# Performance work log

Hardware: AMD Instinct MI355X
Metric: run time of the kernel (lower is better)

The kernel has to match this reference:

```python
import jax, jax.numpy as jnp
import numpy as np

B, S, D, H = 4, 1024, 1024, 16
DH = D // H
K_SPARSE = 32
LAMBDA_MAX, ALPHA = 10.0, 5.0
SPARSE_THRESHOLD = 1.0


def setup_inputs() -> dict:
    key = jax.random.key(0)
    ks = jax.random.split(key, 12)
    x = jax.random.normal(ks[0], (B, S, D), dtype=jnp.float32)
    prior_mask = jax.random.bernoulli(ks[1], 0.1, (S, S))
    prior_indices = jax.random.randint(ks[2], (S, K_SPARSE), 0, S)
    prior_index_mask = jax.random.bernoulli(ks[3], 0.9, (S, K_SPARSE))
    prior_index_mask = prior_index_mask.at[:, 0].set(True)  # avoid all-masked rows
    u_prev = jax.random.normal(ks[4], (B, 1), dtype=jnp.float32)
    sc = 1.0 / np.sqrt(D)
    Wq = jax.random.normal(ks[5], (D, D), dtype=jnp.float32) * sc
    Wk = jax.random.normal(ks[6], (D, D), dtype=jnp.float32) * sc
    Wv = jax.random.normal(ks[7], (D, D), dtype=jnp.float32) * sc
    Wo = jax.random.normal(ks[8], (D, D), dtype=jnp.float32) * sc
    bq = jnp.zeros((D,), jnp.float32)
    bk = jnp.zeros((D,), jnp.float32)
    bv = jnp.zeros((D,), jnp.float32)
    bo = jnp.zeros((D,), jnp.float32)
    return {"x": x, "prior_mask": prior_mask, "prior_indices": prior_indices,
            "prior_index_mask": prior_index_mask, "u_prev": u_prev,
            "Wq": Wq, "bq": bq, "Wk": Wk, "bk": bk, "Wv": Wv, "bv": bv,
            "Wo": Wo, "bo": bo}


def reference(x, prior_mask, prior_indices, prior_index_mask, u_prev,
              Wq, bq, Wk, bk, Wv, bv, Wo, bo):
    Bb, Ss, Dd = x.shape
    scale = 1.0 / jnp.sqrt(jnp.asarray(DH, x.dtype))

    def proj(W, b):
        return (x @ W.T + b).reshape(Bb, Ss, H, DH).transpose(0, 2, 1, 3)  # [B,H,S,DH]

    Q, K, V = proj(Wq, bq), proj(Wk, bk), proj(Wv, bv)

    lam = LAMBDA_MAX * jnp.exp(-ALPHA * u_prev.reshape(Bb))  # [B]
    use_sparse = lam >= SPARSE_THRESHOLD                      # [B] bool

    # ---- dense branch: full SDPA with lambda-scaled prior bias ----
    scores = jnp.einsum('bhqd,bhkd->bhqk', Q, K) * scale      # [B,H,S,S]
    prior_bias = jnp.where(prior_mask[:Ss, :Ss], 0.0, -1.0).astype(x.dtype)
    bias = lam[:, None, None, None] * prior_bias[None, None]
    dense_out = jnp.einsum('bhqk,bhkd->bhqd',
                           jax.nn.softmax(scores + bias, axis=-1), V)

    # ---- sparse branch: gather-indexed SDPA over prior_indices ----
    idx = prior_indices[:Ss]                                   # [S,k]
    Kg = K[:, :, idx]                                          # [B,H,S,k,DH]
    Vg = V[:, :, idx]
    s_scores = jnp.einsum('bhsd,bhskd->bhsk', Q, Kg) * scale   # [B,H,S,k]
    s_scores = jnp.where(prior_index_mask[:Ss][None, None], s_scores,
                         jnp.asarray(-jnp.inf, x.dtype))
    sparse_out = jnp.einsum('bhsk,bhskd->bhsd',
                            jax.nn.softmax(s_scores, axis=-1), Vg)

    out = jnp.where(use_sparse[:, None, None, None], sparse_out, dense_out)
    out = out.transpose(0, 2, 1, 3).reshape(Bb, Ss, Dd)
    return out @ Wo.T + bo
```

## Files before the change

### kernel.cpp

```cpp
#include <hip/hip_runtime.h>
#include <hip/hip_bf16.h>
#include <cmath>

#define NB 4
#define NS 1024
#define ND 1024
#define NH 16
#define NDH 64
#define NKSP 32
#define SCALE 0.125f
#define LOG2E 1.44269504f
#define SCALE2 (SCALE * LOG2E)

typedef __attribute__((ext_vector_type(8))) short bf16x8;
typedef __attribute__((ext_vector_type(4))) float f32x4;
typedef unsigned long long u64;

#define AS1 __attribute__((address_space(1)))
#define AS3 __attribute__((address_space(3)))

__device__ __forceinline__ void gl_lds16(const void* g, void* l) {
    __builtin_amdgcn_global_load_lds((const AS1 void*)g, (AS3 void*)l, 16, 0, 0);
}

__device__ __forceinline__ ushort f2bf(float f) {
    union { __hip_bfloat16 h; ushort u; } cv;
    cv.h = __float2bfloat16(f);
    return cv.u;
}
__device__ __forceinline__ float bf2f(ushort u) {
    union { unsigned int i; float f; } cv;
    cv.i = ((unsigned int)u) << 16;
    return cv.f;
}
__device__ __forceinline__ float fexp2(float x) {
    return __builtin_amdgcn_exp2f(x);
}

__global__ __launch_bounds__(256)
void f2bf_multi(const float* __restrict__ x,
                const float* __restrict__ w0, const float* __restrict__ w1,
                const float* __restrict__ w2, const float* __restrict__ w3,
                const int* __restrict__ pm,
                ushort* __restrict__ xo,
                ushort* __restrict__ o0, ushort* __restrict__ o1,
                ushort* __restrict__ o2, ushort* __restrict__ o3,
                u64* __restrict__ bm)
{
    int y = blockIdx.y;
    if (y == 5) {
        int word = blockIdx.x * 4 + (threadIdx.x >> 6);
        int lane = threadIdx.x & 63;
        int row  = word >> 4, wcol = word & 15;
        int v = pm[(size_t)row * NS + wcol * 64 + lane];
        u64 b = __ballot(v != 0);
        if (lane == 0) bm[word] = b;
        return;
    }
    const float* src; ushort* dst; int nblk;
    if (y == 0)      { src = x;  dst = xo; nblk = 4096; }
    else if (y == 1) { src = w0; dst = o0; nblk = 1024; }
    else if (y == 2) { src = w1; dst = o1; nblk = 1024; }
    else if (y == 3) { src = w2; dst = o2; nblk = 1024; }
    else             { src = w3; dst = o3; nblk = 1024; }
    if (blockIdx.x >= (unsigned)nblk) return;
    int i = (blockIdx.x * 256 + threadIdx.x) * 4;
    float4 v = *(const float4*)&src[i];
    ushort4 o;
    o.x = f2bf(v.x); o.y = f2bf(v.y); o.z = f2bf(v.z); o.w = f2bf(v.w);
    *(ushort4*)&dst[i] = o;
}

__global__ __launch_bounds__(256)
void gemm_qkv(const ushort* __restrict__ xb,
              const ushort* __restrict__ Wqb, const ushort* __restrict__ Wkb,
              const ushort* __restrict__ Wvb,
              const float* __restrict__ bq, const float* __restrict__ bk,
              const float* __restrict__ bv,
              ushort* __restrict__ Qo, ushort* __restrict__ Ko,
              ushort* __restrict__ Vo, ushort* __restrict__ Vto)
{
    constexpr int K = ND;
    __shared__ __attribute__((aligned(16))) ushort As[128 * 32];
    __shared__ __attribute__((aligned(16))) ushort Bs[128 * 32];

    const int tid  = threadIdx.x;
    const int lane = tid & 63, w = tid >> 6;
    const int wm = w >> 1, wn = w & 1;
    const int which = blockIdx.x >> 3;
    const int n0 = (blockIdx.x & 7) * 128;
    const int m0 = blockIdx.y * 128;
    const int quad = lane >> 4, l16 = lane & 15;

    const ushort* W = (which == 0) ? Wqb : (which == 1) ? Wkb : Wvb;
    const float* bias = (which == 0) ? bq : (which == 1) ? bk : bv;
    ushort* Out = (which == 0) ? Qo : (which == 1) ? Ko : Vo;

    f32x4 acc[4][4] = {};

    for (int k0 = 0; k0 < K; k0 += 32) {
        __syncthreads();
#pragma unroll
        for (int u = 0; u < 2; ++u) {
            int t0 = u * 256 + w * 64;
            int t  = t0 + lane;
            int row = t >> 2, kc = (t & 3) * 8;
            gl_lds16(xb + (size_t)(m0 + row) * K + k0 + kc, &As[t0 * 8]);
            gl_lds16(W  + (size_t)(n0 + row) * K + k0 + kc, &Bs[t0 * 8]);
        }
        __syncthreads();

        bf16x8 af[4], bfr[4];
#pragma unroll
        for (int mt = 0; mt < 4; ++mt)
            af[mt] = *(const bf16x8*)&As[(wm*64 + mt*16 + l16) * 32 + quad*8];
#pragma unroll
        for (int nt = 0; nt < 4; ++nt)
            bfr[nt] = *(const bf16x8*)&Bs[(wn*64 + nt*16 + l16) * 32 + quad*8];
#pragma unroll
        for (int mt = 0; mt < 4; ++mt)
#pragma unroll
            for (int nt = 0; nt < 4; ++nt)
                acc[mt][nt] = __builtin_amdgcn_mfma_f32_16x16x32_bf16(
                    af[mt], bfr[nt], acc[mt][nt], 0, 0, 0);
    }

#pragma unroll
    for (int nt = 0; nt < 4; ++nt) {
        int n = n0 + wn*64 + nt*16 + l16;
        float bz = bias[n];
        int hh = n >> 6, dh = n & 63;
#pragma unroll
        for (int mt = 0; mt < 4; ++mt) {
#pragma unroll
            for (int rg = 0; rg < 4; ++rg) {
                int m = m0 + wm*64 + mt*16 + quad*4 + rg;
                int b = m >> 10, s = m & (NS - 1);
                ushort val = f2bf(acc[mt][nt][rg] + bz);
                Out[(((size_t)(b*NH + hh))*NS + s)*NDH + dh] = val;
                if (which == 2)
                    Vto[(((size_t)(b*NH + hh))*NDH + dh)*NS + s] = val;
            }
        }
    }
}

__global__ __launch_bounds__(256)
void gemm_out(const ushort* __restrict__ A, const ushort* __restrict__ W,
              const float* __restrict__ bias, float* __restrict__ Cout)
{
    constexpr int K = ND;
    __shared__ __attribute__((aligned(16))) ushort As[64 * 32];
    __shared__ __attribute__((aligned(16))) ushort Bs[128 * 32];

    const int tid  = threadIdx.x;
    const int lane = tid & 63, w = tid >> 6;
    const int wm = w & 1, wn = w >> 1;
    const int m0 = blockIdx.y * 64, n0 = blockIdx.x * 128;
    const int quad = lane >> 4, l16 = lane & 15;

    f32x4 acc[2][4] = {};

    for (int k0 = 0; k0 < K; k0 += 32) {
        __syncthreads();
        {
            int t0 = w * 64;
            int t  = t0 + lane;
            int row = t >> 2, kc = (t & 3) * 8;
            gl_lds16(A + (size_t)(m0 + row) * K + k0 + kc, &As[t0 * 8]);
        }
#pragma unroll
        for (int u = 0; u < 2; ++u) {
            int t0 = u * 256 + w * 64;
            int t  = t0 + lane;
            int row = t >> 2, kc = (t & 3) * 8;
            gl_lds16(W + (size_t)(n0 + row) * K + k0 + kc, &Bs[t0 * 8]);
        }
        __syncthreads();

        bf16x8 af[2], bfr[4];
#pragma unroll
        for (int mt = 0; mt < 2; ++mt)
            af[mt] = *(const bf16x8*)&As[(wm*32 + mt*16 + l16) * 32 + quad*8];
#pragma unroll
        for (int nt = 0; nt < 4; ++nt)
            bfr[nt] = *(const bf16x8*)&Bs[(wn*64 + nt*16 + l16) * 32 + quad*8];
#pragma unroll
        for (int mt = 0; mt < 2; ++mt)
#pragma unroll
            for (int nt = 0; nt < 4; ++nt)
                acc[mt][nt] = __builtin_amdgcn_mfma_f32_16x16x32_bf16(
                    af[mt], bfr[nt], acc[mt][nt], 0, 0, 0);
    }

#pragma unroll
    for (int nt = 0; nt < 4; ++nt) {
        int n = n0 + wn*64 + nt*16 + l16;
        float bz = bias[n];
#pragma unroll
        for (int mt = 0; mt < 2; ++mt) {
#pragma unroll
            for (int rg = 0; rg < 4; ++rg) {
                int m = m0 + wm*32 + mt*16 + quad*4 + rg;
                Cout[(size_t)m * ND + n] = acc[mt][nt][rg] + bz;
            }
        }
    }
}


#define STAGE(BUF, KT)                                                        \
    _Pragma("unroll")                                                         \
    for (int u = 0; u < 4; ++u) {                                             \
        int cb = w * 256 + u * 64;                                            \
        int c  = cb + lane;                                                   \
        const ushort* src;                                                    \
        if (w < 2) {                                                          \
            int row = c >> 3, sub = c & 7;                                    \
            src = Kh + (((size_t)((KT)*64 + row)) << 6)                       \
                     + ((sub ^ (row & 7)) << 3);                              \
        } else {                                                              \
            int c2 = c - 512;                                                 \
            int row = c2 >> 3, sub = c2 & 7;                                  \
            src = Vth + (size_t)row * NS + (KT)*64                            \
                      + ((sub ^ (row & 7)) << 3);                             \
        }                                                                     \
        gl_lds16(src, (ushort*)&KV[BUF][0][0] + (size_t)cb * 8);              \
    }

#define LOADKV(KF, VF, BUF)                                                   \
    _Pragma("unroll")                                                         \
    for (int nt = 0; nt < 4; ++nt)                                            \
        _Pragma("unroll")                                                     \
        for (int kk = 0; kk < 2; ++kk) {                                      \
            int rowk = nt*16 + l16;                                           \
            int ck = (kk*4 + quad) ^ (l16 & 7);                               \
            KF[nt][kk] = *(const bf16x8*)&KV[BUF][0][rowk*64 + ck*8];         \
            VF[nt][kk] = *(const bf16x8*)&KV[BUF][1][rowk*64 + ck*8];         \
        }

#define STEP(KT, KF, VF)                                                      \
    _Pragma("unroll")                                                         \
    for (int qh = 0; qh < 2; ++qh) {                                          \
        const int qrow = w*32 + qh*16 + l16;                                  \
        u64 wq = MW[(KT)*128 + qrow] >> (quad * 4);                           \
        f32x4 s_acc[4] = {};                                                  \
        __builtin_amdgcn_s_setprio(1);                                        \
        _Pragma("unroll")                                                     \
        for (int nt = 0; nt < 4; ++nt)                                        \
            _Pragma("unroll")                                                 \
            for (int kk = 0; kk < 2; ++kk)                                    \
                s_acc[nt] = __builtin_amdgcn_mfma_f32_16x16x32_bf16(          \
                    KF[nt][kk], qf[qh][kk], s_acc[nt], 0, 0, 0);              \
        __builtin_amdgcn_s_setprio(0);                                        \
        _Pragma("unroll")                                                     \
        for (int nt = 0; nt < 4; ++nt) {                                      \
            ushort4 pk;                                                       \
            float p0 = fexp2(fmaf(s_acc[nt][0], SCALE2,                       \
                 ((wq >> (nt*16 + 0)) & 1ULL) ? 0.f : nlam2));                \
            float p1 = fexp2(fmaf(s_acc[nt][1], SCALE2,                       \
                 ((wq >> (nt*16 + 1)) & 1ULL) ? 0.f : nlam2));                \
            float p2 = fexp2(fmaf(s_acc[nt][2], SCALE2,                       \
                 ((wq >> (nt*16 + 2)) & 1ULL) ? 0.f : nlam2));                \
            float p3 = fexp2(fmaf(s_acc[nt][3], SCALE2,                       \
                 ((wq >> (nt*16 + 3)) & 1ULL) ? 0.f : nlam2));                \
            pk.x = f2bf(p0); pk.y = f2bf(p1);                                 \
            pk.z = f2bf(p2); pk.w = f2bf(p3);                                 \
            *(ushort4*)&Ps[qrow*72 + nt*16 + quad*4] = pk;                    \
        }                                                                     \
        bf16x8 pf[2];                                                         \
        _Pragma("unroll")                                                     \
        for (int kk = 0; kk < 2; ++kk)                                        \
            pf[kk] = *(const bf16x8*)&Ps[qrow*72 + kk*32 + quad*8];           \
        __builtin_amdgcn_s_setprio(1);                                        \
        _Pragma("unroll")                                                     \
        for (int kk = 0; kk < 2; ++kk) {                                      \
            l_acc[qh] = __builtin_amdgcn_mfma_f32_16x16x32_bf16(              \
                pf[kk], ones.v, l_acc[qh], 0, 0, 0);                          \
            _Pragma("unroll")                                                 \
            for (int nt = 0; nt < 4; ++nt)                                    \
                o_acc[qh][nt] = __builtin_amdgcn_mfma_f32_16x16x32_bf16(      \
                    pf[kk], VF[nt][kk], o_acc[qh][nt], 0, 0, 0);              \
        }                                                                     \
        __builtin_amdgcn_s_setprio(0);                                        \
    }

__global__ __launch_bounds__(256, 2)
void attn_kernel(const ushort* __restrict__ Qb, const ushort* __restrict__ Kb,
                 const ushort* __restrict__ Vb, const ushort* __restrict__ Vt,
                 const u64* __restrict__ bm,
                 const int* __restrict__ pidx, const int* __restrict__ pimask,
                 const float* __restrict__ u_prev, ushort* __restrict__ OA)
{
    __shared__ __attribute__((aligned(16))) ushort Ps[128 * 72];
    __shared__ __attribute__((aligned(16))) u64    MW[16 * 128];
    __shared__ __attribute__((aligned(16))) ushort KV[2][2][64 * 64];

    const int tid  = threadIdx.x;
    const int lane = tid & 63, w = tid >> 6;
    const int quad = lane >> 4, l16 = lane & 15;

    const int id    = blockIdx.x;
    const int xcd   = id & 7;
    const int t5    = id >> 3;
    const int qtile = t5 & 7;
    const int head  = (t5 >> 3) * 8 + xcd;
    const int b = head >> 4, h = head & 15;
    const int s0 = qtile * 128;

    const float lam = 10.0f * __expf(-5.0f * u_prev[b]);
    const bool sparse = (lam >= 1.0f);

    const size_t bh = (size_t)b * NH + h;
    const ushort* Qh  = Qb + bh * NS * NDH;
    const ushort* Kh  = Kb + bh * NS * NDH;
    const ushort* Vh  = Vb + bh * NS * NDH;
    const ushort* Vth = Vt + bh * NDH * NS;

    if (!sparse) {
        const float nlam2 = -lam * LOG2E;

        STAGE(0, 0);
#pragma unroll
        for (int u = 0; u < 8; ++u) {
            int idx = u * 256 + tid;
            int row = idx >> 4, wd = idx & 15;
            MW[wd * 128 + row] = bm[(size_t)s0 * 16 + idx];
        }

        bf16x8 qf[2][2];
#pragma unroll
        for (int qh = 0; qh < 2; ++qh)
#pragma unroll
            for (int kk = 0; kk < 2; ++kk)
                qf[qh][kk] = *(const bf16x8*)
                    &Qh[(size_t)(s0 + w*32 + qh*16 + l16) * NDH + kk*32 + quad*8];

        union { bf16x8 v; ushort s[8]; } ones;
#pragma unroll
        for (int i = 0; i < 8; ++i) ones.s[i] = 0x3F80;

        f32x4 o_acc[2][4] = {};
        f32x4 l_acc[2] = {};

        __syncthreads();

        int cur = 0;
        for (int kt = 0; kt < 16; ++kt) {
            if (kt + 1 < 16) STAGE(cur ^ 1, kt + 1);
            bf16x8 kf[4][2], vf[4][2];
            LOADKV(kf, vf, cur);
            STEP(kt, kf, vf);
            __syncthreads();
            cur ^= 1;
        }

#pragma unroll
        for (int qh = 0; qh < 2; ++qh) {
            float inv[4];
#pragma unroll
            for (int rg = 0; rg < 4; ++rg) inv[rg] = 1.f / l_acc[qh][rg];
#pragma unroll
            for (int nt = 0; nt < 4; ++nt)
#pragma unroll
                for (int rg = 0; rg < 4; ++rg) {
                    int m = w*32 + qh*16 + quad*4 + rg;
                    OA[((size_t)b*NS + s0 + m)*ND + h*NDH + nt*16 + l16] =
                        f2bf(o_acc[qh][nt][rg] * inv[rg]);
                }
        }
    } else {
        const int r2  = lane & 15;
        const int cg  = lane >> 4;
#pragma unroll
        for (int qh = 0; qh < 2; ++qh) {
            const int row = w*32 + qh*16 + r2;

            float qreg[64];
            {
                const ushort* qp = Qh + (size_t)(s0 + row) * NDH;
#pragma unroll
                for (int c = 0; c < 8; ++c) {
                    union { bf16x8 v; ushort s[8]; } qv;
                    qv.v = *(const bf16x8*)(qp + c*8);
#pragma unroll
                    for (int j = 0; j < 8; ++j) qreg[c*8 + j] = bf2f(qv.s[j]);
                }
            }

            float sc[8];
#pragma unroll
            for (int jj = 0; jj < 8; ++jj) {
                int j  = cg*8 + jj;
                int mv = pimask[(size_t)(s0+row)*NKSP + j];
                if (mv) {
                    int kv = pidx[(size_t)(s0+row)*NKSP + j];
                    const ushort* krow = &Kh[(size_t)kv * NDH];
                    float acc = 0.f;
#pragma unroll
                    for (int c = 0; c < 8; ++c) {
                        union { bf16x8 v; ushort s[8]; } kk;
                        kk.v = *(const bf16x8*)(krow + c*8);
#pragma unroll
                        for (int jb = 0; jb < 8; ++jb)
                            acc = fmaf(qreg[c*8 + jb], bf2f(kk.s[jb]), acc);
                    }
                    sc[jj] = acc * SCALE;
                } else {
                    sc[jj] = -INFINITY;
                }
            }
            float mt = sc[0];
#pragma unroll
            for (int jj = 1; jj < 8; ++jj) mt = fmaxf(mt, sc[jj]);
            mt = fmaxf(mt, __shfl_xor(mt, 16));
            mt = fmaxf(mt, __shfl_xor(mt, 32));

            float psum = 0.f;
#pragma unroll
            for (int jj = 0; jj < 8; ++jj) {
                float p = __expf(sc[jj] - mt);
                psum += p;
                Ps[row * 72 + cg*8 + jj] = f2bf(p);
            }
            psum += __shfl_xor(psum, 16);
            psum += __shfl_xor(psum, 32);

            float o[16];
#pragma unroll
            for (int i = 0; i < 16; ++i) o[i] = 0.f;

            for (int j = 0; j < 32; ++j) {
                float p = bf2f(Ps[row * 72 + j]);
                if (p != 0.f) {
                    int kv = pidx[(size_t)(s0+row)*NKSP + j];
                    const ushort* vrow = &Vh[(size_t)kv * NDH + cg*16];
#pragma unroll
                    for (int c = 0; c < 2; ++c) {
                        union { bf16x8 v; ushort s[8]; } vv;
                        vv.v = *(const bf16x8*)(vrow + c*8);
#pragma unroll
                        for (int jb = 0; jb < 8; ++jb)
                            o[c*8 + jb] = fmaf(p, bf2f(vv.s[jb]), o[c*8 + jb]);
                    }
                }
            }

            float inv = 1.f / psum;
            ushort* op = OA + ((size_t)b*NS + s0 + row)*ND + h*NDH + cg*16;
#pragma unroll
            for (int i4 = 0; i4 < 4; ++i4) {
                ushort4 v;
                v.x = f2bf(o[i4*4+0]*inv); v.y = f2bf(o[i4*4+1]*inv);
                v.z = f2bf(o[i4*4+2]*inv); v.w = f2bf(o[i4*4+3]*inv);
                *(ushort4*)(op + i4*4) = v;
            }
        }
    }
}

extern "C" void kernel_launch(void* const* d_in, const int* in_sizes, int n_in,
                              void* d_out, int out_size, void* d_ws, size_t ws_size,
                              hipStream_t stream)
{
    const float* x      = (const float*)d_in[0];
    const int*   pmask  = (const int*)  d_in[1];
    const int*   pidx   = (const int*)  d_in[2];
    const int*   pimask = (const int*)  d_in[3];
    const float* u_prev = (const float*)d_in[4];
    const float* Wq     = (const float*)d_in[5];
    const float* bq     = (const float*)d_in[6];
    const float* Wk     = (const float*)d_in[7];
    const float* bk     = (const float*)d_in[8];
    const float* Wv     = (const float*)d_in[9];
    const float* bv     = (const float*)d_in[10];
    const float* Wo     = (const float*)d_in[11];
    const float* bo     = (const float*)d_in[12];
    float* out = (float*)d_out;

    const size_t QSZ = (size_t)NB * NH * NS * NDH;
    const size_t WSZ = (size_t)ND * ND;
    ushort* xb  = (ushort*)d_ws;
    ushort* Qw  = xb  + QSZ;
    ushort* Kw  = Qw  + QSZ;
    ushort* Vw  = Kw  + QSZ;
    ushort* Vtw = Vw  + QSZ;
    ushort* Awb = Vtw + QSZ;
    ushort* Wqb = Awb + QSZ;
    ushort* Wkb = Wqb + WSZ;
    ushort* Wvb = Wkb + WSZ;
    ushort* Wob = Wvb + WSZ;
    u64*    bmw = (u64*)(Wob + WSZ);

    f2bf_multi<<<dim3(4096, 6), 256, 0, stream>>>(
        x, Wq, Wk, Wv, Wo, pmask, xb, Wqb, Wkb, Wvb, Wob, bmw);

    gemm_qkv<<<dim3(24, 32), 256, 0, stream>>>(
        xb, Wqb, Wkb, Wvb, bq, bk, bv, Qw, Kw, Vw, Vtw);

    attn_kernel<<<512, 256, 0, stream>>>(
        Qw, Kw, Vw, Vtw, bmw, pidx, pimask, u_prev, Awb);

    gemm_out<<<dim3(ND/128, (NB*NS)/64), 256, 0, stream>>>(Awb, Wob, bo, out);
}
```

Before: 236.4 us.

## Split attention key range across wave pairs with smaller query tiles

The dense attention kernel now uses 64-row query tiles and 1024 blocks. Within each block the four waves are split into two query groups and two key halves: each key-half wave processes alternate key tiles and the partial O and row-sum accumulators are merged through shared memory at the end. V fragments are now read directly from global memory instead of being staged in LDS, and the sparse branch drops its data-dependent branches in favour of unconditional loads with masking. This raises parallelism and occupancy, at the cost of uncached global V reads, an extra reduction step, and a different block-to-head mapping.

New measurement: 226.0 us. 4.4% less time.

```diff
diff --git a/kernel.cpp b/kernel.cpp
--- a/kernel.cpp
+++ b/kernel.cpp
@@ -209,41 +209,36 @@
 }
 
 
-#define STAGE(BUF, KT)                                                        \
+#define STAGE(BUF, PT)                                                        \
     _Pragma("unroll")                                                         \
     for (int u = 0; u < 4; ++u) {                                             \
         int cb = w * 256 + u * 64;                                            \
         int c  = cb + lane;                                                   \
-        const ushort* src;                                                    \
-        if (w < 2) {                                                          \
-            int row = c >> 3, sub = c & 7;                                    \
-            src = Kh + (((size_t)((KT)*64 + row)) << 6)                       \
-                     + ((sub ^ (row & 7)) << 3);                              \
-        } else {                                                              \
-            int c2 = c - 512;                                                 \
-            int row = c2 >> 3, sub = c2 & 7;                                  \
-            src = Vth + (size_t)row * NS + (KT)*64                            \
-                      + ((sub ^ (row & 7)) << 3);                             \
-        }                                                                     \
-        gl_lds16(src, (ushort*)&KV[BUF][0][0] + (size_t)cb * 8);              \
-    }
-
-#define LOADKV(KF, VF, BUF)                                                   \
+        int wk2 = c >> 9, c2 = c & 511;                                       \
+        int row = c2 >> 3, sub = c2 & 7;                                      \
+        const ushort* src = Kh + (((size_t)(((PT) + wk2)*64 + row)) << 6)     \
+                               + ((sub ^ (row & 7)) << 3);                    \
+        gl_lds16(src, (ushort*)KK + (BUF)*8192 + (size_t)cb * 8);             \
+    }
+
+#define LOADKV(KF, VF, BUF, KT)                                               \
     _Pragma("unroll")                                                         \
     for (int nt = 0; nt < 4; ++nt)                                            \
         _Pragma("unroll")                                                     \
         for (int kk = 0; kk < 2; ++kk) {                                      \
             int rowk = nt*16 + l16;                                           \
             int ck = (kk*4 + quad) ^ (l16 & 7);                               \
-            KF[nt][kk] = *(const bf16x8*)&KV[BUF][0][rowk*64 + ck*8];         \
-            VF[nt][kk] = *(const bf16x8*)&KV[BUF][1][rowk*64 + ck*8];         \
+            KF[nt][kk] = *(const bf16x8*)                                     \
+                &((ushort*)KK)[(BUF)*8192 + wk*4096 + rowk*64 + ck*8];        \
+            VF[nt][kk] = *(const bf16x8*)                                     \
+                &Vth[(size_t)(nt*16 + l16) * NS + (KT)*64 + kk*32 + quad*8];  \
         }
 
 #define STEP(KT, KF, VF)                                                      \
     _Pragma("unroll")                                                         \
     for (int qh = 0; qh < 2; ++qh) {                                          \
-        const int qrow = w*32 + qh*16 + l16;                                  \
-        u64 wq = MW[(KT)*128 + qrow] >> (quad * 4);                           \
+        const int qrow = wq*32 + qh*16 + l16;                                 \
+        u64 wqm = MW[(KT)*64 + qrow] >> (quad * 4);                           \
         f32x4 s_acc[4] = {};                                                  \
         __builtin_amdgcn_s_setprio(1);                                        \
         _Pragma("unroll")                                                     \
@@ -257,21 +252,21 @@
         for (int nt = 0; nt < 4; ++nt) {                                      \
             ushort4 pk;                                                       \
             float p0 = fexp2(fmaf(s_acc[nt][0], SCALE2,                       \
-                 ((wq >> (nt*16 + 0)) & 1ULL) ? 0.f : nlam2));                \
+                 ((wqm >> (nt*16 + 0)) & 1ULL) ? 0.f : nlam2));               \
             float p1 = fexp2(fmaf(s_acc[nt][1], SCALE2,                       \
-                 ((wq >> (nt*16 + 1)) & 1ULL) ? 0.f : nlam2));                \
+                 ((wqm >> (nt*16 + 1)) & 1ULL) ? 0.f : nlam2));               \
             float p2 = fexp2(fmaf(s_acc[nt][2], SCALE2,                       \
-                 ((wq >> (nt*16 + 2)) & 1ULL) ? 0.f : nlam2));                \
+                 ((wqm >> (nt*16 + 2)) & 1ULL) ? 0.f : nlam2));               \
             float p3 = fexp2(fmaf(s_acc[nt][3], SCALE2,                       \
-                 ((wq >> (nt*16 + 3)) & 1ULL) ? 0.f : nlam2));                \
+                 ((wqm >> (nt*16 + 3)) & 1ULL) ? 0.f : nlam2));               \
             pk.x = f2bf(p0); pk.y = f2bf(p1);                                 \
             pk.z = f2bf(p2); pk.w = f2bf(p3);                                 \
-            *(ushort4*)&Ps[qrow*72 + nt*16 + quad*4] = pk;                    \
+            *(ushort4*)&Ps[wk][qrow*72 + nt*16 + quad*4] = pk;                \
         }                                                                     \
         bf16x8 pf[2];                                                         \
         _Pragma("unroll")                                                     \
         for (int kk = 0; kk < 2; ++kk)                                        \
-            pf[kk] = *(const bf16x8*)&Ps[qrow*72 + kk*32 + quad*8];           \
+            pf[kk] = *(const bf16x8*)&Ps[wk][qrow*72 + kk*32 + quad*8];       \
         __builtin_amdgcn_s_setprio(1);                                        \
         _Pragma("unroll")                                                     \
         for (int kk = 0; kk < 2; ++kk) {                                      \
@@ -292,21 +287,22 @@
                  const int* __restrict__ pidx, const int* __restrict__ pimask,
                  const float* __restrict__ u_prev, ushort* __restrict__ OA)
 {
-    __shared__ __attribute__((aligned(16))) ushort Ps[128 * 72];
-    __shared__ __attribute__((aligned(16))) u64    MW[16 * 128];
-    __shared__ __attribute__((aligned(16))) ushort KV[2][2][64 * 64];
+    __shared__ __attribute__((aligned(16))) ushort Ps[2][64 * 72];
+    __shared__ __attribute__((aligned(16))) u64    MW[16 * 64];
+    __shared__ __attribute__((aligned(16))) ushort KK[2][2][64 * 64];
 
     const int tid  = threadIdx.x;
     const int lane = tid & 63, w = tid >> 6;
     const int quad = lane >> 4, l16 = lane & 15;
+    const int wq = w & 1, wk = w >> 1;
 
     const int id    = blockIdx.x;
     const int xcd   = id & 7;
-    const int t5    = id >> 3;
-    const int qtile = t5 & 7;
-    const int head  = (t5 >> 3) * 8 + xcd;
-    const int b = head >> 4, h = head & 15;
-    const int s0 = qtile * 128;
+    const int b     = ((id >> 3) + (id >> 8)) & 3;
+    const int hb    = (id >> 5) & 1;
+    const int qtile = (id >> 6) & 15;
+    const int h     = hb * 8 + xcd;
+    const int s0    = qtile * 64;
 
     const float lam = 10.0f * __expf(-5.0f * u_prev[b]);
     const bool sparse = (lam >= 1.0f);
@@ -322,10 +318,10 @@
 
         STAGE(0, 0);
 #pragma unroll
-        for (int u = 0; u < 8; ++u) {
+        for (int u = 0; u < 4; ++u) {
             int idx = u * 256 + tid;
             int row = idx >> 4, wd = idx & 15;
-            MW[wd * 128 + row] = bm[(size_t)s0 * 16 + idx];
+            MW[wd * 64 + row] = bm[(size_t)s0 * 16 + idx];
         }
 
         bf16x8 qf[2][2];
@@ -334,7 +330,7 @@
 #pragma unroll
             for (int kk = 0; kk < 2; ++kk)
                 qf[qh][kk] = *(const bf16x8*)
-                    &Qh[(size_t)(s0 + w*32 + qh*16 + l16) * NDH + kk*32 + quad*8];
+                    &Qh[(size_t)(s0 + wq*32 + qh*16 + l16) * NDH + kk*32 + quad*8];
 
         union { bf16x8 v; ushort s[8]; } ones;
 #pragma unroll
@@ -346,35 +342,65 @@
         __syncthreads();
 
         int cur = 0;
-        for (int kt = 0; kt < 16; ++kt) {
-            if (kt + 1 < 16) STAGE(cur ^ 1, kt + 1);
+        for (int t = 0; t < 8; ++t) {
+            if (t + 1 < 8) STAGE(cur ^ 1, 2*(t + 1));
             bf16x8 kf[4][2], vf[4][2];
-            LOADKV(kf, vf, cur);
+            const int kt = 2*t + wk;
+            LOADKV(kf, vf, cur, kt);
             STEP(kt, kf, vf);
             __syncthreads();
             cur ^= 1;
         }
 
-#pragma unroll
-        for (int qh = 0; qh < 2; ++qh) {
-            float inv[4];
-#pragma unroll
-            for (int rg = 0; rg < 4; ++rg) inv[rg] = 1.f / l_acc[qh][rg];
-#pragma unroll
-            for (int nt = 0; nt < 4; ++nt)
-#pragma unroll
-                for (int rg = 0; rg < 4; ++rg) {
-                    int m = w*32 + qh*16 + quad*4 + rg;
-                    OA[((size_t)b*NS + s0 + m)*ND + h*NDH + nt*16 + l16] =
-                        f2bf(o_acc[qh][nt][rg] * inv[rg]);
-                }
+        float* POUT = (float*)KK;
+        if (wk == 1) {
+#pragma unroll
+            for (int qh = 0; qh < 2; ++qh) {
+#pragma unroll
+                for (int nt = 0; nt < 4; ++nt)
+#pragma unroll
+                    for (int rg = 0; rg < 4; ++rg)
+                        POUT[(wq*40 + qh*16 + nt*4 + rg)*64 + lane] =
+                            o_acc[qh][nt][rg];
+#pragma unroll
+                for (int rg = 0; rg < 4; ++rg)
+                    POUT[(wq*40 + 32 + qh*4 + rg)*64 + lane] = l_acc[qh][rg];
+            }
+        }
+        __syncthreads();
+        if (wk == 0) {
+#pragma unroll
+            for (int qh = 0; qh < 2; ++qh) {
+#pragma unroll
+                for (int nt = 0; nt < 4; ++nt)
+#pragma unroll
+                    for (int rg = 0; rg < 4; ++rg)
+                        o_acc[qh][nt][rg] +=
+                            POUT[(wq*40 + qh*16 + nt*4 + rg)*64 + lane];
+#pragma unroll
+                for (int rg = 0; rg < 4; ++rg)
+                    l_acc[qh][rg] += POUT[(wq*40 + 32 + qh*4 + rg)*64 + lane];
+            }
+#pragma unroll
+            for (int qh = 0; qh < 2; ++qh) {
+                float inv[4];
+#pragma unroll
+                for (int rg = 0; rg < 4; ++rg) inv[rg] = 1.f / l_acc[qh][rg];
+#pragma unroll
+                for (int nt = 0; nt < 4; ++nt)
+#pragma unroll
+                    for (int rg = 0; rg < 4; ++rg) {
+                        int m = wq*32 + qh*16 + quad*4 + rg;
+                        OA[((size_t)b*NS + s0 + m)*ND + h*NDH + nt*16 + l16] =
+                            f2bf(o_acc[qh][nt][rg] * inv[rg]);
+                    }
+            }
         }
     } else {
         const int r2  = lane & 15;
         const int cg  = lane >> 4;
-#pragma unroll
-        for (int qh = 0; qh < 2; ++qh) {
-            const int row = w*32 + qh*16 + r2;
+        {
+            const int row = w*16 + r2;
 
             float qreg[64];
             {
@@ -393,22 +419,18 @@
             for (int jj = 0; jj < 8; ++jj) {
                 int j  = cg*8 + jj;
                 int mv = pimask[(size_t)(s0+row)*NKSP + j];
-                if (mv) {
-                    int kv = pidx[(size_t)(s0+row)*NKSP + j];
-                    const ushort* krow = &Kh[(size_t)kv * NDH];
-                    float acc = 0.f;
-#pragma unroll
-                    for (int c = 0; c < 8; ++c) {
-                        union { bf16x8 v; ushort s[8]; } kk;
-                        kk.v = *(const bf16x8*)(krow + c*8);
-#pragma unroll
-                        for (int jb = 0; jb < 8; ++jb)
-                            acc = fmaf(qreg[c*8 + jb], bf2f(kk.s[jb]), acc);
-                    }
-                    sc[jj] = acc * SCALE;
-                } else {
-                    sc[jj] = -INFINITY;
+                int kv = pidx[(size_t)(s0+row)*NKSP + j];
+                const ushort* krow = &Kh[(size_t)kv * NDH];
+                float acc = 0.f;
+#pragma unroll
+                for (int c = 0; c < 8; ++c) {
+                    union { bf16x8 v; ushort s[8]; } kk;
+                    kk.v = *(const bf16x8*)(krow + c*8);
+#pragma unroll
+                    for (int jb = 0; jb < 8; ++jb)
+                        acc = fmaf(qreg[c*8 + jb], bf2f(kk.s[jb]), acc);
                 }
+                sc[jj] = mv ? acc * SCALE : -INFINITY;
             }
             float mt = sc[0];
 #pragma unroll
@@ -421,7 +443,7 @@
             for (int jj = 0; jj < 8; ++jj) {
                 float p = __expf(sc[jj] - mt);
                 psum += p;
-                Ps[row * 72 + cg*8 + jj] = f2bf(p);
+                Ps[0][row * 72 + cg*8 + jj] = f2bf(p);
             }
             psum += __shfl_xor(psum, 16);
             psum += __shfl_xor(psum, 32);
@@ -430,19 +452,18 @@
 #pragma unroll
             for (int i = 0; i < 16; ++i) o[i] = 0.f;
 
+#pragma unroll 4
             for (int j = 0; j < 32; ++j) {
-                float p = bf2f(Ps[row * 72 + j]);
-                if (p != 0.f) {
-                    int kv = pidx[(size_t)(s0+row)*NKSP + j];
-                    const ushort* vrow = &Vh[(size_t)kv * NDH + cg*16];
-#pragma unroll
-                    for (int c = 0; c < 2; ++c) {
-                        union { bf16x8 v; ushort s[8]; } vv;
-                        vv.v = *(const bf16x8*)(vrow + c*8);
-#pragma unroll
-                        for (int jb = 0; jb < 8; ++jb)
-                            o[c*8 + jb] = fmaf(p, bf2f(vv.s[jb]), o[c*8 + jb]);
-                    }
+                float p = bf2f(Ps[0][row * 72 + j]);
+                int kv = pidx[(size_t)(s0+row)*NKSP + j];
+                const ushort* vrow = &Vh[(size_t)kv * NDH + cg*16];
+#pragma unroll
+                for (int c = 0; c < 2; ++c) {
+                    union { bf16x8 v; ushort s[8]; } vv;
+                    vv.v = *(const bf16x8*)(vrow + c*8);
+#pragma unroll
+                    for (int jb = 0; jb < 8; ++jb)
+                        o[c*8 + jb] = fmaf(p, bf2f(vv.s[jb]), o[c*8 + jb]);
                 }
             }
 
@@ -498,7 +519,7 @@
     gemm_qkv<<<dim3(24, 32), 256, 0, stream>>>(
         xb, Wqb, Wkb, Wvb, bq, bk, bv, Qw, Kw, Vw, Vtw);
 
-    attn_kernel<<<512, 256, 0, stream>>>(
+    attn_kernel<<<1024, 256, 0, stream>>>(
         Qw, Kw, Vw, Vtw, bmw, pidx, pimask, u_prev, Awb);
 
     gemm_out<<<dim3(ND/128, (NB*NS)/64), 256, 0, stream>>>(Awb, Wob, bo, out);
```
